# Optimization experiments

Hardware: AMD Instinct MI355X
Metric: run time of the kernel (lower is better)

## Reference

```python
import jax, jax.numpy as jnp
import numpy as np

B, T, D, H, A, BIAS_DIM, E = 8, 1024, 1024, 16, 64, 32, 262144  # A = attention_dim_per_head


def setup_inputs() -> dict:
    key = jax.random.key(0)
    ks = jax.random.split(key, 10)
    states = jax.random.normal(ks[0], (B, T, D), dtype=jnp.float32)
    key_states = jax.random.normal(ks[1], (B, T, D), dtype=jnp.float32)
    masks = (jax.random.uniform(ks[2], (B, T, T)) < 0.1).astype(jnp.float32)
    # sparse bias edges: columns (edge_type, batch, query_idx, key_idx)
    et = jax.random.randint(ks[3], (E, 1), 0, BIAS_DIM)
    bi = jax.random.randint(ks[4], (E, 1), 0, B)
    qi = jax.random.randint(ks[5], (E, 1), 0, T)
    ki = jax.random.randint(ks[6], (E, 1), 0, T)
    attention_bias = jnp.concatenate([et, bi, qi, ki], axis=1).astype(jnp.int64)
    # parameters (xavier-like scale)
    def xav(k, shape, fan_in, fan_out):
        a = np.sqrt(6.0 / (fan_in + fan_out))
        return jax.random.uniform(k, shape, minval=-a, maxval=a, dtype=jnp.float32)
    Wq = xav(ks[7], (D, H, A), D, H * A)
    Wk = xav(jax.random.fold_in(ks[7], 1), (D, H, A), D, H * A)
    Wv = xav(jax.random.fold_in(ks[7], 2), (D, H, A), D, H * A)
    Wout = xav(ks[8], (H, A, D), H * A, D)
    bias_embs = xav(ks[9], (BIAS_DIM, A), BIAS_DIM, A)
    bias_scalar = xav(jax.random.fold_in(ks[9], 1), (A, 1), A, 1)
    return {"states": states, "key_states": key_states, "masks": masks,
            "attention_bias": attention_bias, "Wq": Wq, "Wk": Wk, "Wv": Wv,
            "Wout": Wout, "bias_embs": bias_embs, "bias_scalar": bias_scalar}


def reference(states, key_states, masks, attention_bias, Wq, Wk, Wv, Wout, bias_embs, bias_scalar):
    q = jnp.einsum('btd,dha->btha', states, Wq)
    k = jnp.einsum('btd,dha->btha', key_states, Wk)
    v = jnp.einsum('btd,dha->btha', key_states, Wv)
    alpha = jnp.einsum('bkha,bqha->bhqk', k, q)  # [B,H,Q,K]
    # sparse edge bias: embed edge types, project to scalar, scatter into [B,Q,K]
    bvals = (bias_embs[attention_bias[:, 0]] @ bias_scalar)[:, 0]  # [E]
    Bq, Hh, Q, K = alpha.shape
    bs = jnp.zeros((Bq, Q, K), dtype=alpha.dtype).at[
        attention_bias[:, 1], attention_bias[:, 2], attention_bias[:, 3]].set(bvals)
    ksum = k.sum(-1)  # [B,K,H]
    alpha = alpha + jnp.einsum('bqk,bkh->bhqk', bs, ksum)
    alpha = alpha * (1.0 / jnp.sqrt(jnp.float32(A)))
    alpha = alpha - masks[:, None, :, :] * jnp.finfo(jnp.float32).max
    alpha = jax.nn.softmax(alpha, axis=-1)
    context = jnp.einsum('bhqk,bkha->bqha', alpha, v)
    return jnp.einsum('btha,had->btd', context, Wout)
```

## Files before the change

kernel.cpp:

```cpp
#include <hip/hip_runtime.h>
#include <hip/hip_bf16.h>

#define BB 8
#define TT 1024
#define DD 1024
#define HH 16
#define AA 64
#define EE 262144

typedef unsigned short u16;
typedef unsigned int u32;
typedef short bf16x4 __attribute__((ext_vector_type(4)));
typedef short bf16x8 __attribute__((ext_vector_type(8)));
typedef float f32x4 __attribute__((ext_vector_type(4)));

__device__ __forceinline__ float bf2f(u16 u) {
    union { float f; u32 i; } c; c.i = ((u32)u) << 16; return c.f;
}
__device__ __forceinline__ u16 f2bf(float f) {
    union { float f; u32 i; } c; c.f = f;
    u32 x = c.i;
    return (u16)((x + 0x7FFFu + ((x >> 16) & 1u)) >> 16);
}
__device__ __forceinline__ u32 pack2bf(float a, float b) {
    union { __hip_bfloat162 h; u32 u; } c;
    c.h = __float22bfloat162_rn(float2{a, b});
    return c.u;
}

#define GLDS16(gp, lp)                                                        \
    __builtin_amdgcn_global_load_lds(                                         \
        (const __attribute__((address_space(1))) u32*)(const void*)(gp),      \
        (__attribute__((address_space(3))) u32*)(void*)(lp), 16, 0, 0)

#define MFMA(a, b, c) __builtin_amdgcn_mfma_f32_16x16x32_bf16((a), (b), (c), 0, 0, 0)

__global__ __launch_bounds__(256) void cvt(const float* __restrict__ src,
                                           u16* __restrict__ dst) {
    size_t i = ((size_t)blockIdx.x * 256 + threadIdx.x) * 8;
    f32x4 a = *(const f32x4*)(src + i);
    f32x4 b = *(const f32x4*)(src + i + 4);
    u32 o[4];
    o[0] = pack2bf(a[0], a[1]);
    o[1] = pack2bf(a[2], a[3]);
    o[2] = pack2bf(b[0], b[1]);
    o[3] = pack2bf(b[2], b[3]);
    *(bf16x8*)(dst + i) = *(bf16x8*)o;
}

__global__ __launch_bounds__(256) void mbinit(const float* __restrict__ masks,
                                              u16* __restrict__ mb) {
    size_t i = ((size_t)blockIdx.x * 256 + threadIdx.x) * 8;
    f32x4 a = *(const f32x4*)(masks + i);
    f32x4 b = *(const f32x4*)(masks + i + 4);
    const u16 M = f2bf(-1.0e30f);
    bf16x8 o;
#pragma unroll
    for (int j = 0; j < 4; j++) {
        o[j] = (short)((a[j] != 0.f) ? M : 0);
        o[4 + j] = (short)((b[j] != 0.f) ? M : 0);
    }
    *(bf16x8*)(mb + i) = o;
}

__global__ __launch_bounds__(256) void scat_max(const int* __restrict__ ab,
                                                int* __restrict__ idx) {
    int e = blockIdx.x * 256 + threadIdx.x;
    const int* rec = ab + (size_t)e * 4;
    int b = rec[1], q = rec[2], k = rec[3];
    atomicMax(&idx[((((size_t)b << 10) + q) << 10) + k], e);
}

__global__ __launch_bounds__(256) void scat_res(const int* __restrict__ ab,
                                                const int* __restrict__ idx,
                                                const float* __restrict__ be,
                                                const float* __restrict__ bsc,
                                                u16* __restrict__ mb) {
    __shared__ float proj[32];
    int tid = threadIdx.x;
    if (tid < 32) {
        float s = 0.f;
        for (int a = 0; a < 64; a++) s += be[tid * 64 + a] * bsc[a];
        proj[tid] = s * 0.125f;
    }
    __syncthreads();
    int e = blockIdx.x * 256 + tid;
    const int* rec = ab + (size_t)e * 4;
    int et = rec[0], b = rec[1], q = rec[2], k = rec[3];
    size_t cell = ((((size_t)b << 10) + q) << 10) + k;
    if (idx[cell] == e && bf2f(mb[cell]) > -1.0e29f) mb[cell] = f2bf(proj[et]);
}

__global__ __launch_bounds__(256) void tr_w(const float* __restrict__ s0,
                                            const float* __restrict__ s1,
                                            const float* __restrict__ s2,
                                            const float* __restrict__ s3,
                                            u16* __restrict__ dstbase) {
    __shared__ u16 t[64 * 72];
    int tid = threadIdx.x;
    int z = blockIdx.z;
    const float* src = (z == 0) ? s0 : (z == 1) ? s1 : (z == 2) ? s2 : s3;
    u16* dst = dstbase + (size_t)z * 1024 * 1024;
    int row0 = blockIdx.y * 64, col0 = blockIdx.x * 64;
    int r = tid >> 2, c0 = (tid & 3) * 16;
    const float* sp = src + (size_t)(row0 + r) * 1024 + col0 + c0;
    f32x4 f0 = *(const f32x4*)(sp);
    f32x4 f1 = *(const f32x4*)(sp + 4);
    f32x4 f2_ = *(const f32x4*)(sp + 8);
    f32x4 f3 = *(const f32x4*)(sp + 12);
#pragma unroll
    for (int j = 0; j < 4; j++) {
        t[r * 72 + c0 + j] = f2bf(f0[j]);
        t[r * 72 + c0 + 4 + j] = f2bf(f1[j]);
        t[r * 72 + c0 + 8 + j] = f2bf(f2_[j]);
        t[r * 72 + c0 + 12 + j] = f2bf(f3[j]);
    }
    __syncthreads();
    bf16x8 o0, o1;
#pragma unroll
    for (int j = 0; j < 8; j++) o0[j] = (short)t[(c0 + j) * 72 + r];
#pragma unroll
    for (int j = 0; j < 8; j++) o1[j] = (short)t[(c0 + 8 + j) * 72 + r];
    *(bf16x8*)(dst + (size_t)(col0 + r) * 1024 + row0 + c0) = o0;
    *(bf16x8*)(dst + (size_t)(col0 + r) * 1024 + row0 + c0 + 8) = o1;
}

__global__ __launch_bounds__(256) void gemm4(const u16* __restrict__ A,
                                             const u16* __restrict__ BT,
                                             void* __restrict__ C0,
                                             void* __restrict__ C1,
                                             void* __restrict__ C2,
                                             int mode, float sc0) {
    __shared__ u16 Asm[128 * 64];
    __shared__ u16 Bsm[128 * 64];
    int tid = threadIdx.x;
    int wave = tid >> 6, lane = tid & 63;
    int quad = lane >> 4, l16 = lane & 15;
    int wm = wave >> 1, wn = wave & 1;
    int mbase = blockIdx.y * 128, nbase = blockIdx.x * 128;
    f32x4 acc[4][4] = {};
    int srow = wave * 32 + (lane >> 3);
    int schunk = (lane & 7) ^ (lane >> 3);
    const u16* gA = A + (size_t)(mbase + srow) * 1024 + schunk * 8;
    const u16* gB = BT + (size_t)(nbase + srow) * 1024 + schunk * 8;
    u16* lA = Asm + wave * 2048;
    u16* lB = Bsm + wave * 2048;
    int sx = l16 & 7;
    for (int k0 = 0; k0 < 1024; k0 += 64) {
        __syncthreads();
#pragma unroll
        for (int j = 0; j < 4; j++) GLDS16(gA + k0 + j * 8192, lA + j * 512);
#pragma unroll
        for (int j = 0; j < 4; j++) GLDS16(gB + k0 + j * 8192, lB + j * 512);
        __syncthreads();
#pragma unroll
        for (int kk = 0; kk < 2; kk++) {
            bf16x8 af[4], bfr[4];
#pragma unroll
            for (int mt = 0; mt < 4; mt++)
                af[mt] = *(const bf16x8*)&Asm[(wm * 64 + mt * 16 + l16) * 64 +
                                              ((kk * 4 + quad) ^ sx) * 8];
#pragma unroll
            for (int nt = 0; nt < 4; nt++)
                bfr[nt] = *(const bf16x8*)&Bsm[(wn * 64 + nt * 16 + l16) * 64 +
                                               ((kk * 4 + quad) ^ sx) * 8];
#pragma unroll
            for (int mt = 0; mt < 4; mt++)
#pragma unroll
                for (int nt = 0; nt < 4; nt++)
                    acc[mt][nt] = MFMA(af[mt], bfr[nt], acc[mt][nt]);
        }
    }
    if (mode == 0) {
#pragma unroll
        for (int mt = 0; mt < 4; mt++)
#pragma unroll
            for (int nt = 0; nt < 4; nt++)
#pragma unroll
                for (int r = 0; r < 4; r++) {
                    int gm = mbase + wm * 64 + mt * 16 + quad * 4 + r;
                    int gn = nbase + wn * 64 + nt * 16 + l16;
                    ((float*)C0)[(size_t)gm * 1024 + gn] = acc[mt][nt][r];
                }
    } else {
        int mat = nbase >> 10;
        int nloc = nbase & 1023;
        u16* dst = (u16*)((mat == 0) ? C0 : (mat == 1) ? C1 : C2);
        float sc = (mat == 0) ? sc0 : 1.0f;
#pragma unroll
        for (int mt = 0; mt < 4; mt++)
#pragma unroll
            for (int nt = 0; nt < 4; nt++)
#pragma unroll
                for (int r = 0; r < 4; r++) {
                    int gm = mbase + wm * 64 + mt * 16 + quad * 4 + r;
                    int gnl = nloc + wn * 64 + nt * 16 + l16;
                    int b = gm >> 10, t = gm & 1023, h = gnl >> 6, a = gnl & 63;
                    dst[(((size_t)(b * 16 + h) * 1024) + t) * 64 + a] =
                        f2bf(acc[mt][nt][r] * sc);
                }
    }
}

__global__ __launch_bounds__(256) void tr_v(const u16* __restrict__ v,
                                            u16* __restrict__ vT) {
    __shared__ u16 t[64 * 72];
    int tid = threadIdx.x;
    int bh = blockIdx.y;
    int t0 = blockIdx.x * 64;
    int r = tid >> 2, c0 = (tid & 3) * 16;
    const u16* src = v + (size_t)bh * 1024 * 64;
    u16* dst = vT + (size_t)bh * 64 * 1024;
    bf16x8 v0 = *(const bf16x8*)(src + (size_t)(t0 + r) * 64 + c0);
    bf16x8 v1 = *(const bf16x8*)(src + (size_t)(t0 + r) * 64 + c0 + 8);
    *(bf16x8*)&t[r * 72 + c0] = v0;
    *(bf16x8*)&t[r * 72 + c0 + 8] = v1;
    __syncthreads();
    bf16x8 o0, o1;
#pragma unroll
    for (int j = 0; j < 8; j++) o0[j] = (short)t[(c0 + j) * 72 + r];
#pragma unroll
    for (int j = 0; j < 8; j++) o1[j] = (short)t[(c0 + 8 + j) * 72 + r];
    *(bf16x8*)(dst + (size_t)r * 1024 + t0 + c0) = o0;
    *(bf16x8*)(dst + (size_t)r * 1024 + t0 + c0 + 8) = o1;
}

__global__ __launch_bounds__(256) void ksumk(const u16* __restrict__ k,
                                             float* __restrict__ ks) {
    int i = blockIdx.x * 256 + threadIdx.x;
    const u16* kp = k + (size_t)i * 64;
    float s = 0.f;
#pragma unroll
    for (int c = 0; c < 64; c += 8) {
        bf16x8 v = *(const bf16x8*)(kp + c);
#pragma unroll
        for (int j = 0; j < 8; j++) s += bf2f((u16)v[j]);
    }
    ks[i] = s;
}

__global__ __launch_bounds__(256) void attn3(const u16* __restrict__ qbuf,
                                             const u16* __restrict__ kbuf,
                                             const u16* __restrict__ vT,
                                             const float* __restrict__ ksum,
                                             const u16* __restrict__ mb,
                                             u16* __restrict__ ctx) {
    __shared__ u16 Ksm[64 * 72];
    __shared__ u16 Vsm[64 * 72];
    __shared__ u16 Psm[4 * 16 * 72];
    __shared__ float sksm[64];
    __shared__ float lsm[128];
    int tid = threadIdx.x;
    int wave = tid >> 6, lane = tid & 63;
    int quad = lane >> 4, l16 = lane & 15;
    int qb = blockIdx.x, h = blockIdx.y, b = blockIdx.z;
    int bh = b * 16 + h;
    const u16* qp = qbuf + (size_t)bh * 65536;
    const u16* kp = kbuf + (size_t)bh * 65536;
    const u16* vp = vT + (size_t)bh * 65536;
    const float* ksp = ksum + (size_t)bh * 1024;
    int q0w = qb * 128 + wave * 32;
    const u16* mbp[2];
    bf16x8 qf[2][2];
#pragma unroll
    for (int s = 0; s < 2; s++) {
        int qs = q0w + s * 16;
        mbp[s] = mb + ((size_t)b * 1024 + qs + l16) * 1024;
        qf[s][0] = *(const bf16x8*)(qp + (size_t)(qs + l16) * 64 + quad * 8);
        qf[s][1] = *(const bf16x8*)(qp + (size_t)(qs + l16) * 64 + 32 + quad * 8);
    }

    f32x4 oacc[2][4] = {};
    float lsum[2] = {0.f, 0.f};
    int srow = tid >> 2, sc0 = (tid & 3) * 16;
    u16* pw = &Psm[wave * 16 * 72];

    for (int kb = 0; kb < 1024; kb += 64) {
        bf16x8 k0 = *(const bf16x8*)(kp + (size_t)(kb + srow) * 64 + sc0);
        bf16x8 k1 = *(const bf16x8*)(kp + (size_t)(kb + srow) * 64 + sc0 + 8);
        bf16x8 v0 = *(const bf16x8*)(vp + (size_t)srow * 1024 + kb + sc0);
        bf16x8 v1 = *(const bf16x8*)(vp + (size_t)srow * 1024 + kb + sc0 + 8);
        bf16x4 mraw[2][4];
#pragma unroll
        for (int s = 0; s < 2; s++)
#pragma unroll
            for (int nt = 0; nt < 4; nt++)
                mraw[s][nt] = *(const bf16x4*)(mbp[s] + kb + nt * 16 + quad * 4);
        __syncthreads();
        *(bf16x8*)&Ksm[srow * 72 + sc0] = k0;
        *(bf16x8*)&Ksm[srow * 72 + sc0 + 8] = k1;
        *(bf16x8*)&Vsm[srow * 72 + sc0] = v0;
        *(bf16x8*)&Vsm[srow * 72 + sc0 + 8] = v1;
        if (tid < 64) sksm[tid] = ksp[kb + tid];
        __syncthreads();

#pragma unroll
        for (int s = 0; s < 2; s++) {
            f32x4 sacc[4];
#pragma unroll
            for (int nt = 0; nt < 4; nt++) sacc[nt] = f32x4{-20.f, -20.f, -20.f, -20.f};
#pragma unroll
            for (int nt = 0; nt < 4; nt++) {
                bf16x8 kf0 = *(const bf16x8*)&Ksm[(nt * 16 + l16) * 72 + quad * 8];
                bf16x8 kf1 = *(const bf16x8*)&Ksm[(nt * 16 + l16) * 72 + 32 + quad * 8];
                sacc[nt] = MFMA(kf0, qf[s][0], sacc[nt]);
                sacc[nt] = MFMA(kf1, qf[s][1], sacc[nt]);
            }
#pragma unroll
            for (int nt = 0; nt < 4; nt++) {
                f32x4 k4 = *(const f32x4*)&sksm[nt * 16 + quad * 4];
                float p[4];
#pragma unroll
                for (int r = 0; r < 4; r++) {
                    float f = bf2f((u16)mraw[s][nt][r]);
                    float e = __expf(sacc[nt][r] + f * k4[r]);
                    p[r] = (f > -1.0e29f) ? e : 0.f;
                    lsum[s] += p[r];
                }
                *(u32*)&pw[l16 * 72 + nt * 16 + quad * 4] = pack2bf(p[0], p[1]);
                *(u32*)&pw[l16 * 72 + nt * 16 + quad * 4 + 2] = pack2bf(p[2], p[3]);
            }
#pragma unroll
            for (int hs = 0; hs < 2; hs++) {
                bf16x8 pf = *(const bf16x8*)&pw[l16 * 72 + hs * 32 + quad * 8];
#pragma unroll
                for (int at = 0; at < 4; at++) {
                    bf16x8 vf = *(const bf16x8*)&Vsm[(at * 16 + l16) * 72 + hs * 32 + quad * 8];
                    oacc[s][at] = MFMA(pf, vf, oacc[s][at]);
                }
            }
        }
    }

#pragma unroll
    for (int s = 0; s < 2; s++) {
        lsum[s] += __shfl_xor(lsum[s], 16);
        lsum[s] += __shfl_xor(lsum[s], 32);
        if (lane < 16) lsm[wave * 32 + s * 16 + lane] = lsum[s];
    }
    __syncthreads();

#pragma unroll
    for (int s = 0; s < 2; s++)
#pragma unroll
        for (int r = 0; r < 4; r++) {
            float linv = 1.0f / lsm[wave * 32 + s * 16 + quad * 4 + r];
            int q = q0w + s * 16 + quad * 4 + r;
#pragma unroll
            for (int at = 0; at < 4; at++) {
                ctx[(((size_t)b * 1024 + q) * 16 + h) * 64 + at * 16 + l16] =
                    f2bf(oacc[s][at][r] * linv);
            }
        }
}

extern "C" void kernel_launch(void* const* d_in, const int* in_sizes, int n_in,
                              void* d_out, int out_size, void* d_ws, size_t ws_size,
                              hipStream_t stream) {
    const float* states = (const float*)d_in[0];
    const float* key_states = (const float*)d_in[1];
    const float* masks = (const float*)d_in[2];
    const int* abias = (const int*)d_in[3];
    const float* Wq = (const float*)d_in[4];
    const float* Wk = (const float*)d_in[5];
    const float* Wv = (const float*)d_in[6];
    const float* Wout = (const float*)d_in[7];
    const float* be = (const float*)d_in[8];
    const float* bsc = (const float*)d_in[9];

    char* ws = (char*)d_ws;
    size_t off = 0;
    auto alloc = [&](size_t n) { void* p = ws + off; off += (n + 255) & ~(size_t)255; return p; };
    u16* wT = (u16*)alloc(4ull * 1024 * 1024 * 2);
    u16* sbf = (u16*)alloc((size_t)BB * TT * DD * 2);
    u16* kbf = (u16*)alloc((size_t)BB * TT * DD * 2);
    u16* qb_ = (u16*)alloc((size_t)BB * HH * TT * AA * 2);
    u16* kb_ = (u16*)alloc((size_t)BB * HH * TT * AA * 2);
    u16* vb_ = (u16*)alloc((size_t)BB * HH * TT * AA * 2);
    u16* vT_ = (u16*)alloc((size_t)BB * HH * AA * TT * 2);
    float* ks_ = (float*)alloc((size_t)BB * HH * TT * 4);
    u16* mb_ = (u16*)alloc((size_t)BB * TT * TT * 2);

    u16* wqT = wT;
    u16* wkvT = wT + 1048576;
    u16* woT = wT + 3145728;
    int* idx_ = (int*)qb_;
    u16* ctx_ = vb_;

    hipMemsetAsync(idx_, 0xFF, (size_t)BB * TT * TT * 4, stream);
    mbinit<<<dim3(4096), 256, 0, stream>>>(masks, mb_);
    scat_max<<<dim3(EE / 256), 256, 0, stream>>>(abias, idx_);
    scat_res<<<dim3(EE / 256), 256, 0, stream>>>(abias, idx_, be, bsc, mb_);
    tr_w<<<dim3(16, 16, 4), 256, 0, stream>>>(Wq, Wk, Wv, Wout, wT);
    cvt<<<dim3(4096), 256, 0, stream>>>(states, sbf);
    cvt<<<dim3(4096), 256, 0, stream>>>(key_states, kbf);
    gemm4<<<dim3(8, 64), 256, 0, stream>>>(sbf, wqT, qb_, nullptr, nullptr, 1, 0.125f);
    gemm4<<<dim3(16, 64), 256, 0, stream>>>(kbf, wkvT, kb_, vb_, nullptr, 1, 1.0f);
    tr_v<<<dim3(16, 128), 256, 0, stream>>>(vb_, vT_);
    ksumk<<<dim3(512), 256, 0, stream>>>(kb_, ks_);
    attn3<<<dim3(8, 16, 8), 256, 0, stream>>>(qb_, kb_, vT_, ks_, mb_, ctx_);
    gemm4<<<dim3(8, 64), 256, 0, stream>>>(ctx_, woT, d_out, nullptr, nullptr, 0, 1.0f);
}
```

Before: 410.9 us.

## Fuse prep kernels, QKV GEMMs with V-transpose and key-sum, restructure attention tiling

Several independent changes land together. The conversion, mask, index-init and weight-transpose kernels merge into one launch. The Q and K/V projections run as a single GEMM whose epilogue writes V already transposed and computes the per-head key sums, which drops the tr_v and ksumk passes. The attention kernel now uses 64 queries per block instead of 128 and loads K/V tiles through direct global-to-LDS loads into a swizzled layout. The intent is to remove launches and extra memory round trips, at the cost of reloading each K/V tile for twice as many blocks in attention.

```diff
diff --git a/kernel.cpp b/kernel.cpp
--- a/kernel.cpp
+++ b/kernel.cpp
@@ -35,40 +35,86 @@
 
 #define MFMA(a, b, c) __builtin_amdgcn_mfma_f32_16x16x32_bf16((a), (b), (c), 0, 0, 0)
 
-__global__ __launch_bounds__(256) void cvt(const float* __restrict__ src,
-                                           u16* __restrict__ dst) {
-    size_t i = ((size_t)blockIdx.x * 256 + threadIdx.x) * 8;
-    f32x4 a = *(const f32x4*)(src + i);
-    f32x4 b = *(const f32x4*)(src + i + 4);
-    u32 o[4];
-    o[0] = pack2bf(a[0], a[1]);
-    o[1] = pack2bf(a[2], a[3]);
-    o[2] = pack2bf(b[0], b[1]);
-    o[3] = pack2bf(b[2], b[3]);
-    *(bf16x8*)(dst + i) = *(bf16x8*)o;
-}
-
-__global__ __launch_bounds__(256) void mbinit(const float* __restrict__ masks,
-                                              u16* __restrict__ mb) {
-    size_t i = ((size_t)blockIdx.x * 256 + threadIdx.x) * 8;
-    f32x4 a = *(const f32x4*)(masks + i);
-    f32x4 b = *(const f32x4*)(masks + i + 4);
-    const u16 M = f2bf(-1.0e30f);
-    bf16x8 o;
-#pragma unroll
-    for (int j = 0; j < 4; j++) {
-        o[j] = (short)((a[j] != 0.f) ? M : 0);
-        o[4 + j] = (short)((b[j] != 0.f) ? M : 0);
-    }
-    *(bf16x8*)(mb + i) = o;
+__global__ __launch_bounds__(256) void prep1(const float* __restrict__ states,
+                                             const float* __restrict__ keys,
+                                             const float* __restrict__ masks,
+                                             const float* __restrict__ Wq,
+                                             const float* __restrict__ Wk,
+                                             const float* __restrict__ Wv,
+                                             const float* __restrict__ Wout,
+                                             u16* __restrict__ sbf,
+                                             u16* __restrict__ kbf,
+                                             u16* __restrict__ mb,
+                                             int* __restrict__ idx,
+                                             u16* __restrict__ wT) {
+    __shared__ u16 t[64 * 72];
+    int bi = blockIdx.x, tid = threadIdx.x;
+    if (bi < 12288) {
+        if (bi < 8192) {
+            const float* src = (bi < 4096) ? states : keys;
+            u16* dst = (bi < 4096) ? sbf : kbf;
+            size_t i = ((size_t)(bi & 4095) * 256 + tid) * 8;
+            f32x4 a = *(const f32x4*)(src + i);
+            f32x4 b = *(const f32x4*)(src + i + 4);
+            u32 o[4];
+            o[0] = pack2bf(a[0], a[1]);
+            o[1] = pack2bf(a[2], a[3]);
+            o[2] = pack2bf(b[0], b[1]);
+            o[3] = pack2bf(b[2], b[3]);
+            *(bf16x8*)(dst + i) = *(bf16x8*)o;
+        } else {
+            size_t i = ((size_t)(bi - 8192) * 256 + tid) * 8;
+            f32x4 a = *(const f32x4*)(masks + i);
+            f32x4 b = *(const f32x4*)(masks + i + 4);
+            const u16 M = f2bf(-1.0e30f);
+            bf16x8 o;
+#pragma unroll
+            for (int j = 0; j < 4; j++) {
+                o[j] = (short)((a[j] != 0.f) ? M : 0);
+                o[4 + j] = (short)((b[j] != 0.f) ? M : 0);
+            }
+            *(bf16x8*)(mb + i) = o;
+        }
+    } else if (bi < 16384) {
+        size_t i = ((size_t)(bi - 12288) * 256 + tid) * 8;
+        int4 m1 = {-1, -1, -1, -1};
+        *(int4*)(idx + i) = m1;
+        *(int4*)(idx + i + 4) = m1;
+    } else {
+        int zb = bi - 16384;
+        int z = zb >> 8, by = (zb >> 4) & 15, bx = zb & 15;
+        const float* src = (z == 0) ? Wq : (z == 1) ? Wk : (z == 2) ? Wv : Wout;
+        u16* dst = wT + (size_t)z * 1048576;
+        int row0 = by * 64, col0 = bx * 64;
+        int r = tid >> 2, c0 = (tid & 3) * 16;
+        const float* sp = src + (size_t)(row0 + r) * 1024 + col0 + c0;
+        f32x4 f0 = *(const f32x4*)(sp);
+        f32x4 f1 = *(const f32x4*)(sp + 4);
+        f32x4 f2_ = *(const f32x4*)(sp + 8);
+        f32x4 f3 = *(const f32x4*)(sp + 12);
+#pragma unroll
+        for (int j = 0; j < 4; j++) {
+            t[r * 72 + c0 + j] = f2bf(f0[j]);
+            t[r * 72 + c0 + 4 + j] = f2bf(f1[j]);
+            t[r * 72 + c0 + 8 + j] = f2bf(f2_[j]);
+            t[r * 72 + c0 + 12 + j] = f2bf(f3[j]);
+        }
+        __syncthreads();
+        bf16x8 o0, o1;
+#pragma unroll
+        for (int j = 0; j < 8; j++) o0[j] = (short)t[(c0 + j) * 72 + r];
+#pragma unroll
+        for (int j = 0; j < 8; j++) o1[j] = (short)t[(c0 + 8 + j) * 72 + r];
+        *(bf16x8*)(dst + (size_t)(col0 + r) * 1024 + row0 + c0) = o0;
+        *(bf16x8*)(dst + (size_t)(col0 + r) * 1024 + row0 + c0 + 8) = o1;
+    }
 }
 
 __global__ __launch_bounds__(256) void scat_max(const int* __restrict__ ab,
                                                 int* __restrict__ idx) {
     int e = blockIdx.x * 256 + threadIdx.x;
-    const int* rec = ab + (size_t)e * 4;
-    int b = rec[1], q = rec[2], k = rec[3];
-    atomicMax(&idx[((((size_t)b << 10) + q) << 10) + k], e);
+    int4 rec = ((const int4*)ab)[e];
+    atomicMax(&idx[((((size_t)rec.y << 10) + rec.z) << 10) + rec.w], e);
 }
 
 __global__ __launch_bounds__(256) void scat_res(const int* __restrict__ ab,
@@ -85,52 +131,229 @@
     }
     __syncthreads();
     int e = blockIdx.x * 256 + tid;
-    const int* rec = ab + (size_t)e * 4;
-    int et = rec[0], b = rec[1], q = rec[2], k = rec[3];
-    size_t cell = ((((size_t)b << 10) + q) << 10) + k;
-    if (idx[cell] == e && bf2f(mb[cell]) > -1.0e29f) mb[cell] = f2bf(proj[et]);
-}
-
-__global__ __launch_bounds__(256) void tr_w(const float* __restrict__ s0,
-                                            const float* __restrict__ s1,
-                                            const float* __restrict__ s2,
-                                            const float* __restrict__ s3,
-                                            u16* __restrict__ dstbase) {
-    __shared__ u16 t[64 * 72];
+    int4 rec = ((const int4*)ab)[e];
+    size_t cell = ((((size_t)rec.y << 10) + rec.z) << 10) + rec.w;
+    if (idx[cell] == e && bf2f(mb[cell]) > -1.0e29f) mb[cell] = f2bf(proj[rec.x]);
+}
+
+__global__ __launch_bounds__(256) void gemm5(const u16* __restrict__ sbf,
+                                             const u16* __restrict__ kbf,
+                                             const u16* __restrict__ wT,
+                                             u16* __restrict__ qb,
+                                             u16* __restrict__ kb,
+                                             u16* __restrict__ vT,
+                                             float* __restrict__ ks) {
+    __shared__ u16 smem[17408];
     int tid = threadIdx.x;
-    int z = blockIdx.z;
-    const float* src = (z == 0) ? s0 : (z == 1) ? s1 : (z == 2) ? s2 : s3;
-    u16* dst = dstbase + (size_t)z * 1024 * 1024;
-    int row0 = blockIdx.y * 64, col0 = blockIdx.x * 64;
-    int r = tid >> 2, c0 = (tid & 3) * 16;
-    const float* sp = src + (size_t)(row0 + r) * 1024 + col0 + c0;
-    f32x4 f0 = *(const f32x4*)(sp);
-    f32x4 f1 = *(const f32x4*)(sp + 4);
-    f32x4 f2_ = *(const f32x4*)(sp + 8);
-    f32x4 f3 = *(const f32x4*)(sp + 12);
-#pragma unroll
-    for (int j = 0; j < 4; j++) {
-        t[r * 72 + c0 + j] = f2bf(f0[j]);
-        t[r * 72 + c0 + 4 + j] = f2bf(f1[j]);
-        t[r * 72 + c0 + 8 + j] = f2bf(f2_[j]);
-        t[r * 72 + c0 + 12 + j] = f2bf(f3[j]);
-    }
+    int wave = tid >> 6, lane = tid & 63;
+    int quad = lane >> 4, l16 = lane & 15;
+    int wm = wave >> 1, wn = wave & 1;
+    int mat = blockIdx.x >> 3;
+    int nloc = (blockIdx.x & 7) * 128;
+    int mbase = blockIdx.y * 128;
+    const u16* A = (mat == 0) ? sbf : kbf;
+    const u16* BT = wT + (size_t)mat * 1048576;
+    u16* Asm = smem;
+    u16* Bsm = smem + 8192;
+    f32x4 acc[4][4] = {};
+    int srow = wave * 32 + (lane >> 3);
+    int schunk = (lane & 7) ^ (lane >> 3);
+    const u16* gA = A + (size_t)(mbase + srow) * 1024 + schunk * 8;
+    const u16* gB = BT + (size_t)(nloc + srow) * 1024 + schunk * 8;
+    u16* lA = Asm + wave * 2048;
+    u16* lB = Bsm + wave * 2048;
+    int sx = l16 & 7;
+    for (int k0 = 0; k0 < 1024; k0 += 64) {
+        __syncthreads();
+#pragma unroll
+        for (int j = 0; j < 4; j++) GLDS16(gA + k0 + j * 8192, lA + j * 512);
+#pragma unroll
+        for (int j = 0; j < 4; j++) GLDS16(gB + k0 + j * 8192, lB + j * 512);
+        __syncthreads();
+#pragma unroll
+        for (int kk = 0; kk < 2; kk++) {
+            bf16x8 af[4], bfr[4];
+#pragma unroll
+            for (int mt = 0; mt < 4; mt++)
+                af[mt] = *(const bf16x8*)&Asm[(wm * 64 + mt * 16 + l16) * 64 +
+                                              ((kk * 4 + quad) ^ sx) * 8];
+#pragma unroll
+            for (int nt = 0; nt < 4; nt++)
+                bfr[nt] = *(const bf16x8*)&Bsm[(wn * 64 + nt * 16 + l16) * 64 +
+                                               ((kk * 4 + quad) ^ sx) * 8];
+#pragma unroll
+            for (int mt = 0; mt < 4; mt++)
+#pragma unroll
+                for (int nt = 0; nt < 4; nt++)
+                    acc[mt][nt] = MFMA(af[mt], bfr[nt], acc[mt][nt]);
+        }
+    }
+
+    if (mat == 2) {
+        __syncthreads();
+#pragma unroll
+        for (int mt = 0; mt < 4; mt++)
+#pragma unroll
+            for (int nt = 0; nt < 4; nt++)
+#pragma unroll
+                for (int r = 0; r < 4; r++) {
+                    int rowl = wm * 64 + mt * 16 + quad * 4 + r;
+                    int coll = wn * 64 + nt * 16 + l16;
+                    smem[coll * 136 + rowl] = f2bf(acc[mt][nt][r]);
+                }
+        __syncthreads();
+        int b = mbase >> 10, t0 = mbase & 1023;
+        int c = tid >> 1, hf = tid & 1;
+        int h = (nloc >> 6) + (c >> 6);
+        int a = c & 63;
+        u16* dst = vT + ((((size_t)(b * 16 + h)) * 64 + a) << 10) + t0 + hf * 64;
+        const u16* srcl = smem + c * 136 + hf * 64;
+#pragma unroll
+        for (int j = 0; j < 8; j++) *(bf16x8*)(dst + j * 8) = *(const bf16x8*)(srcl + j * 8);
+    } else {
+        u16* dst = (mat == 0) ? qb : kb;
+        float sc = (mat == 0) ? 0.125f : 1.0f;
+#pragma unroll
+        for (int mt = 0; mt < 4; mt++)
+#pragma unroll
+            for (int nt = 0; nt < 4; nt++)
+#pragma unroll
+                for (int r = 0; r < 4; r++) {
+                    int gm = mbase + wm * 64 + mt * 16 + quad * 4 + r;
+                    int gnl = nloc + wn * 64 + nt * 16 + l16;
+                    int b = gm >> 10, t = gm & 1023, h = gnl >> 6, a = gnl & 63;
+                    dst[(((size_t)(b * 16 + h) * 1024) + t) * 64 + a] =
+                        f2bf(acc[mt][nt][r] * sc);
+                }
+        if (mat == 1) {
+            int h = (nloc + wn * 64) >> 6;
+#pragma unroll
+            for (int mt = 0; mt < 4; mt++)
+#pragma unroll
+                for (int r = 0; r < 4; r++) {
+                    float s = acc[mt][0][r] + acc[mt][1][r] + acc[mt][2][r] + acc[mt][3][r];
+                    s += __shfl_xor(s, 1);
+                    s += __shfl_xor(s, 2);
+                    s += __shfl_xor(s, 4);
+                    s += __shfl_xor(s, 8);
+                    if (l16 == 0) {
+                        int gm = mbase + wm * 64 + mt * 16 + quad * 4 + r;
+                        int b = gm >> 10, t = gm & 1023;
+                        ks[(((size_t)(b * 16 + h)) << 10) + t] = s;
+                    }
+                }
+        }
+    }
+}
+
+__global__ __launch_bounds__(256) void attn4(const u16* __restrict__ qbuf,
+                                             const u16* __restrict__ kbuf,
+                                             const u16* __restrict__ vT,
+                                             const float* __restrict__ ksum,
+                                             const u16* __restrict__ mb,
+                                             u16* __restrict__ ctx) {
+    __shared__ u16 Ksm[64 * 64];
+    __shared__ u16 Vsm[64 * 64];
+    __shared__ u16 Psm[4 * 16 * 72];
+    __shared__ float sksm[64];
+    __shared__ float lsm[64];
+    int tid = threadIdx.x;
+    int wave = tid >> 6, lane = tid & 63;
+    int quad = lane >> 4, l16 = lane & 15;
+    int qb = blockIdx.x, h = blockIdx.y, b = blockIdx.z;
+    int bh = b * 16 + h;
+    const u16* qp = qbuf + (size_t)bh * 65536;
+    const u16* kp = kbuf + (size_t)bh * 65536;
+    const u16* vp = vT + (size_t)bh * 65536;
+    const float* ksp = ksum + (size_t)bh * 1024;
+    int q0 = qb * 64 + wave * 16;
+    const u16* mbp = mb + ((size_t)b * 1024 + q0 + l16) * 1024;
+
+    bf16x8 qf0 = *(const bf16x8*)(qp + (size_t)(q0 + l16) * 64 + quad * 8);
+    bf16x8 qf1 = *(const bf16x8*)(qp + (size_t)(q0 + l16) * 64 + 32 + quad * 8);
+
+    f32x4 oacc[4] = {};
+    float lsum = 0.f;
+    int r8 = lane >> 3;
+    int sch = (lane & 7) ^ r8;
+    u16* lK = Ksm + wave * 1024;
+    u16* lV = Vsm + wave * 1024;
+    const u16* gK0 = kp + (size_t)(wave * 16 + r8) * 64 + sch * 8;
+    const u16* gV0 = vp + (size_t)(wave * 16 + r8) * 1024 + sch * 8;
+    int sx = l16 & 7;
+    u16* pw = &Psm[wave * 16 * 72];
+
+    for (int kb = 0; kb < 1024; kb += 64) {
+        bf16x4 mraw[4];
+#pragma unroll
+        for (int nt = 0; nt < 4; nt++)
+            mraw[nt] = *(const bf16x4*)(mbp + kb + nt * 16 + quad * 4);
+        __syncthreads();
+        GLDS16(gK0 + (size_t)kb * 64, lK);
+        GLDS16(gK0 + (size_t)(kb + 8) * 64, lK + 512);
+        GLDS16(gV0 + kb, lV);
+        GLDS16(gV0 + 8 * 1024 + kb, lV + 512);
+        if (tid < 64) sksm[tid] = ksp[kb + tid];
+        __syncthreads();
+
+        f32x4 sacc[4];
+#pragma unroll
+        for (int nt = 0; nt < 4; nt++) sacc[nt] = f32x4{-20.f, -20.f, -20.f, -20.f};
+#pragma unroll
+        for (int nt = 0; nt < 4; nt++) {
+            bf16x8 kf0 = *(const bf16x8*)&Ksm[(nt * 16 + l16) * 64 + (quad ^ sx) * 8];
+            bf16x8 kf1 = *(const bf16x8*)&Ksm[(nt * 16 + l16) * 64 + ((4 + quad) ^ sx) * 8];
+            sacc[nt] = MFMA(kf0, qf0, sacc[nt]);
+            sacc[nt] = MFMA(kf1, qf1, sacc[nt]);
+        }
+
+#pragma unroll
+        for (int nt = 0; nt < 4; nt++) {
+            f32x4 k4 = *(const f32x4*)&sksm[nt * 16 + quad * 4];
+            float p[4];
+#pragma unroll
+            for (int r = 0; r < 4; r++) {
+                float f = bf2f((u16)mraw[nt][r]);
+                float e = __expf(sacc[nt][r] + f * k4[r]);
+                p[r] = (f > -1.0e29f) ? e : 0.f;
+                lsum += p[r];
+            }
+            *(u32*)&pw[l16 * 72 + nt * 16 + quad * 4] = pack2bf(p[0], p[1]);
+            *(u32*)&pw[l16 * 72 + nt * 16 + quad * 4 + 2] = pack2bf(p[2], p[3]);
+        }
+
+#pragma unroll
+        for (int hs = 0; hs < 2; hs++) {
+            bf16x8 pf = *(const bf16x8*)&pw[l16 * 72 + hs * 32 + quad * 8];
+#pragma unroll
+            for (int at = 0; at < 4; at++) {
+                bf16x8 vf = *(const bf16x8*)&Vsm[(at * 16 + l16) * 64 +
+                                                 ((hs * 4 + quad) ^ sx) * 8];
+                oacc[at] = MFMA(pf, vf, oacc[at]);
+            }
+        }
+    }
+
+    lsum += __shfl_xor(lsum, 16);
+    lsum += __shfl_xor(lsum, 32);
+    if (lane < 16) lsm[wave * 16 + lane] = lsum;
     __syncthreads();
-    bf16x8 o0, o1;
-#pragma unroll
-    for (int j = 0; j < 8; j++) o0[j] = (short)t[(c0 + j) * 72 + r];
-#pragma unroll
-    for (int j = 0; j < 8; j++) o1[j] = (short)t[(c0 + 8 + j) * 72 + r];
-    *(bf16x8*)(dst + (size_t)(col0 + r) * 1024 + row0 + c0) = o0;
-    *(bf16x8*)(dst + (size_t)(col0 + r) * 1024 + row0 + c0 + 8) = o1;
-}
-
-__global__ __launch_bounds__(256) void gemm4(const u16* __restrict__ A,
+
+#pragma unroll
+    for (int r = 0; r < 4; r++) {
+        float linv = 1.0f / lsm[wave * 16 + quad * 4 + r];
+        int q = q0 + quad * 4 + r;
+#pragma unroll
+        for (int at = 0; at < 4; at++) {
+            ctx[(((size_t)b * 1024 + q) * 16 + h) * 64 + at * 16 + l16] =
+                f2bf(oacc[at][r] * linv);
+        }
+    }
+}
+
+__global__ __launch_bounds__(256) void gemmo(const u16* __restrict__ A,
                                              const u16* __restrict__ BT,
-                                             void* __restrict__ C0,
-                                             void* __restrict__ C1,
-                                             void* __restrict__ C2,
-                                             int mode, float sc0) {
+                                             float* __restrict__ C) {
     __shared__ u16 Asm[128 * 64];
     __shared__ u16 Bsm[128 * 64];
     int tid = threadIdx.x;
@@ -171,187 +394,16 @@
                     acc[mt][nt] = MFMA(af[mt], bfr[nt], acc[mt][nt]);
         }
     }
-    if (mode == 0) {
-#pragma unroll
-        for (int mt = 0; mt < 4; mt++)
-#pragma unroll
-            for (int nt = 0; nt < 4; nt++)
-#pragma unroll
-                for (int r = 0; r < 4; r++) {
-                    int gm = mbase + wm * 64 + mt * 16 + quad * 4 + r;
-                    int gn = nbase + wn * 64 + nt * 16 + l16;
-                    ((float*)C0)[(size_t)gm * 1024 + gn] = acc[mt][nt][r];
-                }
-    } else {
-        int mat = nbase >> 10;
-        int nloc = nbase & 1023;
-        u16* dst = (u16*)((mat == 0) ? C0 : (mat == 1) ? C1 : C2);
-        float sc = (mat == 0) ? sc0 : 1.0f;
-#pragma unroll
-        for (int mt = 0; mt < 4; mt++)
-#pragma unroll
-            for (int nt = 0; nt < 4; nt++)
-#pragma unroll
-                for (int r = 0; r < 4; r++) {
-                    int gm = mbase + wm * 64 + mt * 16 + quad * 4 + r;
-                    int gnl = nloc + wn * 64 + nt * 16 + l16;
-                    int b = gm >> 10, t = gm & 1023, h = gnl >> 6, a = gnl & 63;
-                    dst[(((size_t)(b * 16 + h) * 1024) + t) * 64 + a] =
-                        f2bf(acc[mt][nt][r] * sc);
-                }
-    }
-}
-
-__global__ __launch_bounds__(256) void tr_v(const u16* __restrict__ v,
-                                            u16* __restrict__ vT) {
-    __shared__ u16 t[64 * 72];
-    int tid = threadIdx.x;
-    int bh = blockIdx.y;
-    int t0 = blockIdx.x * 64;
-    int r = tid >> 2, c0 = (tid & 3) * 16;
-    const u16* src = v + (size_t)bh * 1024 * 64;
-    u16* dst = vT + (size_t)bh * 64 * 1024;
-    bf16x8 v0 = *(const bf16x8*)(src + (size_t)(t0 + r) * 64 + c0);
-    bf16x8 v1 = *(const bf16x8*)(src + (size_t)(t0 + r) * 64 + c0 + 8);
-    *(bf16x8*)&t[r * 72 + c0] = v0;
-    *(bf16x8*)&t[r * 72 + c0 + 8] = v1;
-    __syncthreads();
-    bf16x8 o0, o1;
-#pragma unroll
-    for (int j = 0; j < 8; j++) o0[j] = (short)t[(c0 + j) * 72 + r];
-#pragma unroll
-    for (int j = 0; j < 8; j++) o1[j] = (short)t[(c0 + 8 + j) * 72 + r];
-    *(bf16x8*)(dst + (size_t)r * 1024 + t0 + c0) = o0;
-    *(bf16x8*)(dst + (size_t)r * 1024 + t0 + c0 + 8) = o1;
-}
-
-__global__ __launch_bounds__(256) void ksumk(const u16* __restrict__ k,
-                                             float* __restrict__ ks) {
-    int i = blockIdx.x * 256 + threadIdx.x;
-    const u16* kp = k + (size_t)i * 64;
-    float s = 0.f;
-#pragma unroll
-    for (int c = 0; c < 64; c += 8) {
-        bf16x8 v = *(const bf16x8*)(kp + c);
-#pragma unroll
-        for (int j = 0; j < 8; j++) s += bf2f((u16)v[j]);
-    }
-    ks[i] = s;
-}
-
-__global__ __launch_bounds__(256) void attn3(const u16* __restrict__ qbuf,
-                                             const u16* __restrict__ kbuf,
-                                             const u16* __restrict__ vT,
-                                             const float* __restrict__ ksum,
-                                             const u16* __restrict__ mb,
-                                             u16* __restrict__ ctx) {
-    __shared__ u16 Ksm[64 * 72];
-    __shared__ u16 Vsm[64 * 72];
-    __shared__ u16 Psm[4 * 16 * 72];
-    __shared__ float sksm[64];
-    __shared__ float lsm[128];
-    int tid = threadIdx.x;
-    int wave = tid >> 6, lane = tid & 63;
-    int quad = lane >> 4, l16 = lane & 15;
-    int qb = blockIdx.x, h = blockIdx.y, b = blockIdx.z;
-    int bh = b * 16 + h;
-    const u16* qp = qbuf + (size_t)bh * 65536;
-    const u16* kp = kbuf + (size_t)bh * 65536;
-    const u16* vp = vT + (size_t)bh * 65536;
-    const float* ksp = ksum + (size_t)bh * 1024;
-    int q0w = qb * 128 + wave * 32;
-    const u16* mbp[2];
-    bf16x8 qf[2][2];
-#pragma unroll
-    for (int s = 0; s < 2; s++) {
-        int qs = q0w + s * 16;
-        mbp[s] = mb + ((size_t)b * 1024 + qs + l16) * 1024;
-        qf[s][0] = *(const bf16x8*)(qp + (size_t)(qs + l16) * 64 + quad * 8);
-        qf[s][1] = *(const bf16x8*)(qp + (size_t)(qs + l16) * 64 + 32 + quad * 8);
-    }
-
-    f32x4 oacc[2][4] = {};
-    float lsum[2] = {0.f, 0.f};
-    int srow = tid >> 2, sc0 = (tid & 3) * 16;
-    u16* pw = &Psm[wave * 16 * 72];
-
-    for (int kb = 0; kb < 1024; kb += 64) {
-        bf16x8 k0 = *(const bf16x8*)(kp + (size_t)(kb + srow) * 64 + sc0);
-        bf16x8 k1 = *(const bf16x8*)(kp + (size_t)(kb + srow) * 64 + sc0 + 8);
-        bf16x8 v0 = *(const bf16x8*)(vp + (size_t)srow * 1024 + kb + sc0);
-        bf16x8 v1 = *(const bf16x8*)(vp + (size_t)srow * 1024 + kb + sc0 + 8);
-        bf16x4 mraw[2][4];
-#pragma unroll
-        for (int s = 0; s < 2; s++)
-#pragma unroll
-            for (int nt = 0; nt < 4; nt++)
-                mraw[s][nt] = *(const bf16x4*)(mbp[s] + kb + nt * 16 + quad * 4);
-        __syncthreads();
-        *(bf16x8*)&Ksm[srow * 72 + sc0] = k0;
-        *(bf16x8*)&Ksm[srow * 72 + sc0 + 8] = k1;
-        *(bf16x8*)&Vsm[srow * 72 + sc0] = v0;
-        *(bf16x8*)&Vsm[srow * 72 + sc0 + 8] = v1;
-        if (tid < 64) sksm[tid] = ksp[kb + tid];
-        __syncthreads();
-
-#pragma unroll
-        for (int s = 0; s < 2; s++) {
-            f32x4 sacc[4];
-#pragma unroll
-            for (int nt = 0; nt < 4; nt++) sacc[nt] = f32x4{-20.f, -20.f, -20.f, -20.f};
-#pragma unroll
-            for (int nt = 0; nt < 4; nt++) {
-                bf16x8 kf0 = *(const bf16x8*)&Ksm[(nt * 16 + l16) * 72 + quad * 8];
-                bf16x8 kf1 = *(const bf16x8*)&Ksm[(nt * 16 + l16) * 72 + 32 + quad * 8];
-                sacc[nt] = MFMA(kf0, qf[s][0], sacc[nt]);
-                sacc[nt] = MFMA(kf1, qf[s][1], sacc[nt]);
+#pragma unroll
+    for (int mt = 0; mt < 4; mt++)
+#pragma unroll
+        for (int nt = 0; nt < 4; nt++)
+#pragma unroll
+            for (int r = 0; r < 4; r++) {
+                int gm = mbase + wm * 64 + mt * 16 + quad * 4 + r;
+                int gn = nbase + wn * 64 + nt * 16 + l16;
+                C[(size_t)gm * 1024 + gn] = acc[mt][nt][r];
             }
-#pragma unroll
-            for (int nt = 0; nt < 4; nt++) {
-                f32x4 k4 = *(const f32x4*)&sksm[nt * 16 + quad * 4];
-                float p[4];
-#pragma unroll
-                for (int r = 0; r < 4; r++) {
-                    float f = bf2f((u16)mraw[s][nt][r]);
-                    float e = __expf(sacc[nt][r] + f * k4[r]);
-                    p[r] = (f > -1.0e29f) ? e : 0.f;
-                    lsum[s] += p[r];
-                }
-                *(u32*)&pw[l16 * 72 + nt * 16 + quad * 4] = pack2bf(p[0], p[1]);
-                *(u32*)&pw[l16 * 72 + nt * 16 + quad * 4 + 2] = pack2bf(p[2], p[3]);
-            }
-#pragma unroll
-            for (int hs = 0; hs < 2; hs++) {
-                bf16x8 pf = *(const bf16x8*)&pw[l16 * 72 + hs * 32 + quad * 8];
-#pragma unroll
-                for (int at = 0; at < 4; at++) {
-                    bf16x8 vf = *(const bf16x8*)&Vsm[(at * 16 + l16) * 72 + hs * 32 + quad * 8];
-                    oacc[s][at] = MFMA(pf, vf, oacc[s][at]);
-                }
-            }
-        }
-    }
-
-#pragma unroll
-    for (int s = 0; s < 2; s++) {
-        lsum[s] += __shfl_xor(lsum[s], 16);
-        lsum[s] += __shfl_xor(lsum[s], 32);
-        if (lane < 16) lsm[wave * 32 + s * 16 + lane] = lsum[s];
-    }
-    __syncthreads();
-
-#pragma unroll
-    for (int s = 0; s < 2; s++)
-#pragma unroll
-        for (int r = 0; r < 4; r++) {
-            float linv = 1.0f / lsm[wave * 32 + s * 16 + quad * 4 + r];
-            int q = q0w + s * 16 + quad * 4 + r;
-#pragma unroll
-            for (int at = 0; at < 4; at++) {
-                ctx[(((size_t)b * 1024 + q) * 16 + h) * 64 + at * 16 + l16] =
-                    f2bf(oacc[s][at][r] * linv);
-            }
-        }
 }
 
 extern "C" void kernel_launch(void* const* d_in, const int* in_sizes, int n_in,
@@ -376,28 +428,19 @@
     u16* kbf = (u16*)alloc((size_t)BB * TT * DD * 2);
     u16* qb_ = (u16*)alloc((size_t)BB * HH * TT * AA * 2);
     u16* kb_ = (u16*)alloc((size_t)BB * HH * TT * AA * 2);
-    u16* vb_ = (u16*)alloc((size_t)BB * HH * TT * AA * 2);
     u16* vT_ = (u16*)alloc((size_t)BB * HH * AA * TT * 2);
     float* ks_ = (float*)alloc((size_t)BB * HH * TT * 4);
     u16* mb_ = (u16*)alloc((size_t)BB * TT * TT * 2);
 
-    u16* wqT = wT;
-    u16* wkvT = wT + 1048576;
     u16* woT = wT + 3145728;
     int* idx_ = (int*)qb_;
-    u16* ctx_ = vb_;
-
-    hipMemsetAsync(idx_, 0xFF, (size_t)BB * TT * TT * 4, stream);
-    mbinit<<<dim3(4096), 256, 0, stream>>>(masks, mb_);
+    u16* ctx_ = sbf;
+
+    prep1<<<dim3(17408), 256, 0, stream>>>(states, key_states, masks, Wq, Wk, Wv,
+                                           Wout, sbf, kbf, mb_, idx_, wT);
     scat_max<<<dim3(EE / 256), 256, 0, stream>>>(abias, idx_);
     scat_res<<<dim3(EE / 256), 256, 0, stream>>>(abias, idx_, be, bsc, mb_);
-    tr_w<<<dim3(16, 16, 4), 256, 0, stream>>>(Wq, Wk, Wv, Wout, wT);
-    cvt<<<dim3(4096), 256, 0, stream>>>(states, sbf);
-    cvt<<<dim3(4096), 256, 0, stream>>>(key_states, kbf);
-    gemm4<<<dim3(8, 64), 256, 0, stream>>>(sbf, wqT, qb_, nullptr, nullptr, 1, 0.125f);
-    gemm4<<<dim3(16, 64), 256, 0, stream>>>(kbf, wkvT, kb_, vb_, nullptr, 1, 1.0f);
-    tr_v<<<dim3(16, 128), 256, 0, stream>>>(vb_, vT_);
-    ksumk<<<dim3(512), 256, 0, stream>>>(kb_, ks_);
-    attn3<<<dim3(8, 16, 8), 256, 0, stream>>>(qb_, kb_, vT_, ks_, mb_, ctx_);
-    gemm4<<<dim3(8, 64), 256, 0, stream>>>(ctx_, woT, d_out, nullptr, nullptr, 0, 1.0f);
-}
+    gemm5<<<dim3(24, 64), 256, 0, stream>>>(sbf, kbf, wT, qb_, kb_, vT_, ks_);
+    attn4<<<dim3(16, 16, 8), 256, 0, stream>>>(qb_, kb_, vT_, ks_, mb_, ctx_);
+    gemmo<<<dim3(8, 64), 256, 0, stream>>>(ctx_, woT, (float*)d_out);
+}
```

Result: faster. 371.6 us (-9.6%).
